# Optimization experiments

Measured on AMD Instinct MI355X. Metric: run time of the kernel, lower is better.

## Reference

```python
import jax, jax.numpy as jnp
import numpy as np

LN_EPS = 1e-5


def _layernorm(x, g, b):
    mu = x.mean(-1, keepdims=True)
    var = x.var(-1, keepdims=True)
    return (x - mu) / jnp.sqrt(var + LN_EPS) * g + b


def _rel_pos_index(p):
    # static numpy computation, identical to the torch buffer
    coords = np.stack(np.meshgrid(np.arange(p), np.arange(p), indexing='ij'))  # (2,p,p)
    flat = coords.reshape(2, -1)  # (2, p*p)
    rel = flat[:, :, None] - flat[:, None, :]  # (2, N, N)
    rel = rel.transpose(1, 2, 0).copy()
    rel[:, :, 0] += p - 1
    rel[:, :, 1] += p - 1
    rel[:, :, 0] *= 2 * p - 1
    return rel.sum(-1)  # (N, N)


def setup_inputs() -> dict:
    key = jax.random.key(0)
    ks = jax.random.split(key, 8)
    B, H, W, C, heads, p = 32, 56, 56, 384, 12, 7
    hid = 4 * C
    s = 0.02
    return {
        'x': jax.random.normal(ks[0], (B, H * W, C), jnp.float32),
        'norm1_g': jnp.ones((C,), jnp.float32),
        'norm1_b': jnp.zeros((C,), jnp.float32),
        'qkv_w': jax.random.normal(ks[1], (3 * C, C), jnp.float32) * s,
        'qkv_b': jnp.zeros((3 * C,), jnp.float32),
        'rpb_table': jax.random.normal(ks[2], ((2 * p - 1) ** 2, heads), jnp.float32) * s,
        'proj_w': jax.random.normal(ks[3], (C, C), jnp.float32) * s,
        'proj_b': jnp.zeros((C,), jnp.float32),
        'norm2_g': jnp.ones((C,), jnp.float32),
        'norm2_b': jnp.zeros((C,), jnp.float32),
        'fc1_w': jax.random.normal(ks[4], (hid, C), jnp.float32) * s,
        'fc1_b': jnp.zeros((hid,), jnp.float32),
        'fc2_w': jax.random.normal(ks[5], (C, hid), jnp.float32) * s,
        'fc2_b': jnp.zeros((C,), jnp.float32),
        'H': H, 'W': W, 'patch_size': p, 'num_heads': heads,
    }


def reference(x, norm1_g, norm1_b, qkv_w, qkv_b, rpb_table, proj_w, proj_b,
              norm2_g, norm2_b, fc1_w, fc1_b, fc2_w, fc2_b,
              H, W, patch_size, num_heads):
    B, L, C = x.shape
    p = patch_size
    N = p * p
    head_dim = C // num_heads
    scale = head_dim ** -0.5

    shortcut = x
    h = _layernorm(x, norm1_g, norm1_b).reshape(B, H, W, C)
    # partition into (B*nWin, N, C); H, W divisible by p so no padding
    h = h.reshape(B, H // p, p, W // p, p, C).transpose(0, 1, 3, 2, 4, 5)
    patches = h.reshape(-1, N, C)
    Bw = patches.shape[0]

    # IPSA attention
    qkv = patches @ qkv_w.T + qkv_b  # (Bw, N, 3C)
    qkv = qkv.reshape(Bw, N, 3, num_heads, head_dim).transpose(2, 0, 3, 1, 4)
    q, k, v = qkv[0] * scale, qkv[1], qkv[2]  # (Bw, h, N, d)
    attn = jnp.einsum('bhnd,bhmd->bhnm', q, k)
    bias = rpb_table[_rel_pos_index(p).reshape(-1)].reshape(N, N, num_heads)
    attn = attn + bias.transpose(2, 0, 1)[None]
    attn = jax.nn.softmax(attn, axis=-1)
    out = jnp.einsum('bhnm,bhmd->bhnd', attn, v).transpose(0, 2, 1, 3).reshape(Bw, N, C)
    out = out @ proj_w.T + proj_b

    # reverse partition
    out = out.reshape(B, H // p, W // p, p, p, C).transpose(0, 1, 3, 2, 4, 5)
    out = out.reshape(B, H * W, C)

    x = shortcut + out
    y = _layernorm(x, norm2_g, norm2_b)
    y = jax.nn.gelu(y @ fc1_w.T + fc1_b, approximate=False)
    y = y @ fc2_w.T + fc2_b
    return x + y
```

## Files before the change

### kernel.cpp

```cpp
#include <hip/hip_runtime.h>
#include <cstdint>
#include <cstddef>

typedef __bf16 bf16;
typedef __bf16 bf16x4 __attribute__((ext_vector_type(4)));
typedef __bf16 bf16x8 __attribute__((ext_vector_type(8)));
typedef float f32x4 __attribute__((ext_vector_type(4)));

static_assert(sizeof(bf16x8) == 16, "bf16x8 must be 16B");

#define NTOK 100352
#define CDIM 384

#define AS1(p) ((const __attribute__((address_space(1))) void*)(p))
#define AS3(p) ((__attribute__((address_space(3))) void*)(p))

__global__ __launch_bounds__(256) void cvt_k(const float* __restrict__ in,
                                             bf16* __restrict__ out, int n)
{
    const int i = (blockIdx.x * 256 + threadIdx.x) * 4;
    if (i < n) {
        const float4 v = *(const float4*)(in + i);
        bf16x4 o;
        o[0] = (bf16)v.x; o[1] = (bf16)v.y; o[2] = (bf16)v.z; o[3] = (bf16)v.w;
        *(bf16x4*)(out + i) = o;
    }
}

__global__ __launch_bounds__(256) void bias_k(const float* __restrict__ rpb,
                                              float* __restrict__ biasE)
{
    const int t = blockIdx.x * 256 + threadIdx.x;
    const int i = t & 63, j = (t >> 6) & 63, hd = t >> 12;
    float v = -3e38f;
    if (i < 49 && j < 49) {
        const int iy = i / 7, ix = i % 7, jy = j / 7, jx = j % 7;
        v = rpb[((jy - iy + 6) * 13 + (jx - ix + 6)) * 12 + hd];
    }
    biasE[t] = v;
}

__global__ __launch_bounds__(256) void ln32_k(const float* __restrict__ x,
    const float* __restrict__ g, const float* __restrict__ b, bf16* __restrict__ y)
{
    const int wave = threadIdx.x >> 6, lane = threadIdx.x & 63;
    const size_t row = (size_t)blockIdx.x * 4 + wave;
    const float2* xr = (const float2*)(x + row * CDIM);
    float v[6];
    float s = 0.f, s2 = 0.f;
#pragma unroll
    for (int i = 0; i < 3; i++) {
        const float2 t = xr[lane + i * 64];
        v[2 * i] = t.x; v[2 * i + 1] = t.y;
        s += t.x + t.y; s2 += t.x * t.x + t.y * t.y;
    }
#pragma unroll
    for (int off = 32; off > 0; off >>= 1) {
        s  += __shfl_xor(s, off);
        s2 += __shfl_xor(s2, off);
    }
    const float mu   = s * (1.f / CDIM);
    const float rstd = rsqrtf(s2 * (1.f / CDIM) - mu * mu + 1e-5f);
    const float2* gu = (const float2*)g;
    const float2* bu = (const float2*)b;
    uint32_t* yu = (uint32_t*)(y + row * CDIM);
#pragma unroll
    for (int i = 0; i < 3; i++) {
        const float2 gg = gu[lane + i * 64], bb = bu[lane + i * 64];
        const float o0 = (v[2 * i] - mu) * rstd * gg.x + bb.x;
        const float o1 = (v[2 * i + 1] - mu) * rstd * gg.y + bb.y;
        const uint32_t pk = (uint32_t)__builtin_bit_cast(unsigned short, (bf16)o0)
                          | ((uint32_t)__builtin_bit_cast(unsigned short, (bf16)o1) << 16);
        yu[lane + i * 64] = pk;
    }
}

template <int EPI, typename TO>
__global__ __launch_bounds__(256) void gemm_bt(
    const bf16* __restrict__ A, const bf16* __restrict__ Bm,
    const float* __restrict__ bias, const float* __restrict__ res,
    TO* __restrict__ Cc, int N, int K)
{
    __shared__ __align__(16) bf16 lds[2][2][128 * 32];
    const int tid = threadIdx.x;

    const int gx = gridDim.x;
    const int nwg = gx * gridDim.y;
    const int orig = blockIdx.y * gx + blockIdx.x;
    const int q = nwg >> 3, r = nwg & 7;
    const int xcd = orig & 7, lid = orig >> 3;
    const int swz = (xcd < r ? xcd * (q + 1) : r * (q + 1) + (xcd - r) * q) + lid;
    const int m0 = (swz / gx) * 128, n0 = (swz % gx) * 128;

    const int wave = tid >> 6, lane = tid & 63;
    const int wm = (wave >> 1) * 64, wn = (wave & 1) * 64;
    const int lm = lane & 15, lk = (lane >> 4) * 8;

    const int sr = tid >> 2;
    const int sc = (tid & 3) * 8;

    const bf16* Ap0 = A + (size_t)(m0 + sr) * K + sc;
    const bf16* Ap1 = A + (size_t)(m0 + sr + 64) * K + sc;
    const bf16* Bp0 = Bm + (size_t)(n0 + sr) * K + sc;
    const bf16* Bp1 = Bm + (size_t)(n0 + sr + 64) * K + sc;

#define STAGE(buf, koff) do {                                                           \
    __builtin_amdgcn_global_load_lds(AS1(Ap0 + (koff)),                                 \
        AS3(&lds[buf][0][(wave * 16) * 32]), 16, 0, 0);                                 \
    __builtin_amdgcn_global_load_lds(AS1(Ap1 + (koff)),                                 \
        AS3(&lds[buf][0][(64 + wave * 16) * 32]), 16, 0, 0);                            \
    __builtin_amdgcn_global_load_lds(AS1(Bp0 + (koff)),                                 \
        AS3(&lds[buf][1][(wave * 16) * 32]), 16, 0, 0);                                 \
    __builtin_amdgcn_global_load_lds(AS1(Bp1 + (koff)),                                 \
        AS3(&lds[buf][1][(64 + wave * 16) * 32]), 16, 0, 0);                            \
} while (0)

    f32x4 acc[4][4] = {};

    const int nt = K >> 5;
    STAGE(0, 0);
    __syncthreads();
    int cur = 0;
    for (int t = 0; t < nt; ++t) {
        const bool more = (t + 1 < nt);
        if (more) STAGE(cur ^ 1, (t + 1) << 5);
        bf16x8 af[4], bfr[4];
#pragma unroll
        for (int i = 0; i < 4; i++)
            af[i] = *(const bf16x8*)&lds[cur][0][(wm + i * 16 + lm) * 32 + lk];
#pragma unroll
        for (int i = 0; i < 4; i++)
            bfr[i] = *(const bf16x8*)&lds[cur][1][(wn + i * 16 + lm) * 32 + lk];
#pragma unroll
        for (int mi = 0; mi < 4; mi++)
#pragma unroll
            for (int ni = 0; ni < 4; ni++)
                acc[mi][ni] = __builtin_amdgcn_mfma_f32_16x16x32_bf16(
                    af[mi], bfr[ni], acc[mi][ni], 0, 0, 0);
        if (more) { __syncthreads(); cur ^= 1; }
    }
#undef STAGE

    if (EPI == 2) {
        const int rb = m0 + wm + (lane >> 4) * 4;
        const int cb = n0 + wn + lm;
#pragma unroll
        for (int ni = 0; ni < 4; ni++) {
            const int col = cb + ni * 16;
            const float bv = bias[col];
#pragma unroll
            for (int mi = 0; mi < 4; mi++) {
#pragma unroll
                for (int r2 = 0; r2 < 4; r2++) {
                    const int row = rb + mi * 16 + r2;
                    float v = acc[mi][ni][r2] + bv;
                    v += res[(size_t)row * N + col];
                    Cc[(size_t)row * N + col] = (TO)v;
                }
            }
        }
    } else {
        __syncthreads();
        bf16* Ct = (bf16*)lds;
        const int rbl = wm + (lane >> 4) * 4;
        const int cbl = wn + lm;
#pragma unroll
        for (int ni = 0; ni < 4; ni++) {
            const float bv = bias[n0 + cbl + ni * 16];
#pragma unroll
            for (int mi = 0; mi < 4; mi++) {
#pragma unroll
                for (int r2 = 0; r2 < 4; r2++) {
                    float v = acc[mi][ni][r2] + bv;
                    if (EPI == 1) {
                        const float p  = fmaf(v * v, 0.07135481627f, 1.59576912161f);
                        const float u2 = fminf(v * p, 80.f);
                        const float e  = __expf(u2);
                        v = v * e * __builtin_amdgcn_rcpf(1.f + e);
                    }
                    Ct[(rbl + mi * 16 + r2) * 128 + cbl + ni * 16] = (bf16)v;
                }
            }
        }
        __syncthreads();
#pragma unroll
        for (int c2 = 0; c2 < 8; ++c2) {
            const int chunk = tid + (c2 << 8);
            const int row = chunk >> 4, c8 = (chunk & 15) << 3;
            *(bf16x8*)((bf16*)Cc + (size_t)(m0 + row) * N + n0 + c8) =
                *(const bf16x8*)&Ct[row * 128 + c8];
        }
    }
}

__global__ __launch_bounds__(256) void attn_k(const bf16* __restrict__ qkv,
    const float* __restrict__ biasE, bf16* __restrict__ out)
{
    const int w  = blockIdx.x;
    const int bb = w >> 6, win = w & 63, wy = win >> 3, wx = win & 7;
    __shared__ int toks[64];
    __shared__ __align__(16) bf16 VT[4][32 * 64];
    __shared__ __align__(16) bf16 P[4][64 * 64];
    const int tid = threadIdx.x;
    if (tid < 64) {
        const int t = tid < 49 ? tid : 48;
        toks[tid] = bb * 3136 + (wy * 7 + t / 7) * 56 + wx * 7 + t % 7;
    }
    __syncthreads();

    const int wave = tid >> 6, lane = tid & 63;
    const int g = lane >> 4, lr = lane & 15;
    char* vt = (char*)VT[wave];
    char* pb = (char*)P[wave];

    for (int hh = 0; hh < 3; ++hh) {
        const int hd = wave * 3 + hh;
#pragma unroll
        for (int c = 0; c < 4; ++c) {
            const int idx = c * 64 + lane;
            const int row = idx >> 2, d0 = (idx & 3) * 8;
            if (row < 49) {
                const bf16x8 vv = *(const bf16x8*)(qkv + (size_t)toks[row] * 1152 + 768 + hd * 32 + d0);
#pragma unroll
                for (int e = 0; e < 8; ++e) {
                    const int d = d0 + e;
                    *(bf16*)(vt + (((d * 64 + row) * 2) ^ ((d & 7) << 4))) = vv[e];
                }
            } else {
#pragma unroll
                for (int e = 0; e < 8; ++e) {
                    const int d = d0 + e;
                    *(bf16*)(vt + (((d * 64 + row) * 2) ^ ((d & 7) << 4))) = (bf16)0.f;
                }
            }
        }
        bf16x8 kf[4], qf[4];
#pragma unroll
        for (int b = 0; b < 4; ++b) {
            const size_t rk = (size_t)toks[b * 16 + lr] * 1152;
            kf[b] = *(const bf16x8*)(qkv + rk + 384 + hd * 32 + g * 8);
            qf[b] = *(const bf16x8*)(qkv + rk +       hd * 32 + g * 8);
        }
        f32x4 s[4][4] = {};
#pragma unroll
        for (int mi = 0; mi < 4; ++mi)
#pragma unroll
            for (int nj = 0; nj < 4; ++nj)
                s[mi][nj] = __builtin_amdgcn_mfma_f32_16x16x32_bf16(kf[mi], qf[nj], s[mi][nj], 0, 0, 0);
        const float* bh = biasE + hd * 4096;
#pragma unroll
        for (int nj = 0; nj < 4; ++nj) {
            const int j = nj * 16 + lr;
            const float* bj = bh + j * 64 + g * 4;
            float mx = -3e38f;
#pragma unroll
            for (int mi = 0; mi < 4; ++mi) {
                const float4 be = *(const float4*)(bj + mi * 16);
                const float* bp4 = (const float*)&be;
#pragma unroll
                for (int r2 = 0; r2 < 4; ++r2) {
                    const float v = fmaf(s[mi][nj][r2], 0.1767766952966369f, bp4[r2]);
                    s[mi][nj][r2] = v;
                    mx = fmaxf(mx, v);
                }
            }
            mx = fmaxf(mx, __shfl_xor(mx, 16));
            mx = fmaxf(mx, __shfl_xor(mx, 32));
            float sm = 0.f;
#pragma unroll
            for (int mi = 0; mi < 4; ++mi)
#pragma unroll
                for (int r2 = 0; r2 < 4; ++r2) {
                    const float e = __expf(s[mi][nj][r2] - mx);
                    s[mi][nj][r2] = e;
                    sm += e;
                }
            sm += __shfl_xor(sm, 16);
            sm += __shfl_xor(sm, 32);
            const float inv = __builtin_amdgcn_rcpf(sm);
#pragma unroll
            for (int mi = 0; mi < 4; ++mi) {
                bf16x4 pk;
#pragma unroll
                for (int r2 = 0; r2 < 4; ++r2) pk[r2] = (bf16)(s[mi][nj][r2] * inv);
                const int i0 = mi * 16 + g * 4;
                *(bf16x4*)(pb + (((j * 64 + i0) * 2) ^ ((j & 7) << 4))) = pk;
            }
        }
        f32x4 o[2][4] = {};
#pragma unroll
        for (int kb = 0; kb < 2; ++kb) {
            bf16x8 av[2], bp[4];
#pragma unroll
            for (int db = 0; db < 2; ++db) {
                const int d = db * 16 + lr;
                av[db] = *(const bf16x8*)(vt + (((d * 64 + kb * 32 + g * 8) * 2) ^ ((d & 7) << 4)));
            }
#pragma unroll
            for (int jb = 0; jb < 4; ++jb) {
                const int j = jb * 16 + lr;
                bp[jb] = *(const bf16x8*)(pb + (((j * 64 + kb * 32 + g * 8) * 2) ^ ((j & 7) << 4)));
            }
#pragma unroll
            for (int db = 0; db < 2; ++db)
#pragma unroll
                for (int jb = 0; jb < 4; ++jb)
                    o[db][jb] = __builtin_amdgcn_mfma_f32_16x16x32_bf16(av[db], bp[jb], o[db][jb], 0, 0, 0);
        }
#pragma unroll
        for (int jb = 0; jb < 4; ++jb) {
            const int j = jb * 16 + lr;
            if (j < 49) {
                bf16* op = out + (size_t)toks[j] * CDIM + hd * 32 + g * 4;
#pragma unroll
                for (int db = 0; db < 2; ++db) {
                    bf16x4 pk;
#pragma unroll
                    for (int r2 = 0; r2 < 4; ++r2) pk[r2] = (bf16)o[db][jb][r2];
                    *(bf16x4*)(op + db * 16) = pk;
                }
            }
        }
    }
}

extern "C" void kernel_launch(void* const* d_in, const int* in_sizes, int n_in,
                              void* d_out, int out_size, void* d_ws, size_t ws_size,
                              hipStream_t stream) {
    const float* x      = (const float*)d_in[0];
    const float* n1g    = (const float*)d_in[1];
    const float* n1b    = (const float*)d_in[2];
    const float* qkv_w  = (const float*)d_in[3];
    const float* qkv_b  = (const float*)d_in[4];
    const float* rpb    = (const float*)d_in[5];
    const float* proj_w = (const float*)d_in[6];
    const float* proj_b = (const float*)d_in[7];
    const float* n2g    = (const float*)d_in[8];
    const float* n2b    = (const float*)d_in[9];
    const float* fc1_w  = (const float*)d_in[10];
    const float* fc1_b  = (const float*)d_in[11];
    const float* fc2_w  = (const float*)d_in[12];
    const float* fc2_b  = (const float*)d_in[13];
    float* out = (float*)d_out;

    const size_t wBytes = 3538944 + 196608;
    int nc = 16;
    for (int c : {1, 2, 4, 8}) {
        if (wBytes + ((size_t)NTOK / c) * 3840 <= ws_size) { nc = c; break; }
    }
    const int rowsC = NTOK / nc;
    const int imgsC = 32 / nc;

    char* ws = (char*)d_ws;
    bf16* wqkv  = (bf16*)ws;
    bf16* wproj = wqkv + 442368;
    bf16* wfc1  = wproj + 147456;
    bf16* wfc2  = wfc1 + 589824;
    float* biasE = (float*)(ws + 3538944);
    bf16* bufH  = (bf16*)(ws + wBytes);
    bf16* bufB  = bufH + (size_t)rowsC * CDIM;
    float* x1   = out;

    cvt_k<<<442368 / 1024, 256, 0, stream>>>(qkv_w, wqkv, 442368);
    cvt_k<<<147456 / 1024, 256, 0, stream>>>(proj_w, wproj, 147456);
    cvt_k<<<589824 / 1024, 256, 0, stream>>>(fc1_w, wfc1, 589824);
    cvt_k<<<589824 / 1024, 256, 0, stream>>>(fc2_w, wfc2, 589824);
    bias_k<<<192, 256, 0, stream>>>(rpb, biasE);

    for (int c = 0; c < nc; c++) {
        const size_t ro = (size_t)c * rowsC;
        ln32_k<<<rowsC / 4, 256, 0, stream>>>(x + ro * CDIM, n1g, n1b, bufH);
        gemm_bt<0, bf16><<<dim3(1152 / 128, rowsC / 128), 256, 0, stream>>>(
            bufH, wqkv, qkv_b, nullptr, bufB, 1152, 384);
        attn_k<<<dim3(64 * imgsC), 256, 0, stream>>>(bufB, biasE, bufH);
        gemm_bt<2, float><<<dim3(384 / 128, rowsC / 128), 256, 0, stream>>>(
            bufH, wproj, proj_b, x + ro * CDIM, x1 + ro * CDIM, 384, 384);
    }
    for (int c = 0; c < nc; c++) {
        const size_t ro = (size_t)c * rowsC;
        ln32_k<<<rowsC / 4, 256, 0, stream>>>(x1 + ro * CDIM, n2g, n2b, bufH);
        gemm_bt<1, bf16><<<dim3(1536 / 128, rowsC / 128), 256, 0, stream>>>(
            bufH, wfc1, fc1_b, nullptr, bufB, 1536, 384);
        gemm_bt<2, float><<<dim3(384 / 128, rowsC / 128), 256, 0, stream>>>(
            bufB, wfc2, fc2_b, x1 + ro * CDIM, out + ro * CDIM, 384, 1536);
    }
}
```

Before: 1.116 ms.

## Triple-buffer GEMM LDS staging with XOR swizzle to avoid bank conflicts

Moves the bf16 GEMM from double to triple buffering in LDS. Loads are issued two K-tiles ahead, and explicit vmcnt waits plus raw s_barrier replace __syncthreads. It also XOR-swizzles the 16-byte column chunks within each LDS row, on both the global_load_lds write and the fragment read, to reduce LDS bank conflicts. The aim is to hide global load latency and cut LDS read stalls, at the cost of 50% more LDS per block (possible occupancy loss) and hand-tuned waitcnt counts that must match the loads issued.

```diff
diff --git a/kernel.cpp b/kernel.cpp
--- a/kernel.cpp
+++ b/kernel.cpp
@@ -81,7 +81,7 @@
     const float* __restrict__ bias, const float* __restrict__ res,
     TO* __restrict__ Cc, int N, int K)
 {
-    __shared__ __align__(16) bf16 lds[2][2][128 * 32];
+    __shared__ __align__(16) bf16 lds[3][2][128 * 32];
     const int tid = threadIdx.x;
 
     const int gx = gridDim.x;
@@ -94,10 +94,11 @@
 
     const int wave = tid >> 6, lane = tid & 63;
     const int wm = (wave >> 1) * 64, wn = (wave & 1) * 64;
-    const int lm = lane & 15, lk = (lane >> 4) * 8;
+    const int lm = lane & 15;
+    const int lko = (((lane >> 4) ^ ((lm >> 1) & 3)) & 3) * 8;
 
     const int sr = tid >> 2;
-    const int sc = (tid & 3) * 8;
+    const int sc = (((tid & 3) ^ ((sr >> 1) & 3)) & 3) * 8;
 
     const bf16* Ap0 = A + (size_t)(m0 + sr) * K + sc;
     const bf16* Ap1 = A + (size_t)(m0 + sr + 64) * K + sc;
@@ -119,25 +120,38 @@
 
     const int nt = K >> 5;
     STAGE(0, 0);
-    __syncthreads();
-    int cur = 0;
+    STAGE(1, 32);
+    int bi = 0;
     for (int t = 0; t < nt; ++t) {
-        const bool more = (t + 1 < nt);
-        if (more) STAGE(cur ^ 1, (t + 1) << 5);
+        if (t + 2 < nt) {
+            const int b2 = bi ? bi - 1 : 2;
+            STAGE(b2, (t + 2) << 5);
+            asm volatile("s_waitcnt vmcnt(8)" ::: "memory");
+        } else if (t + 1 < nt) {
+            asm volatile("s_waitcnt vmcnt(4)" ::: "memory");
+        } else {
+            asm volatile("s_waitcnt vmcnt(0)" ::: "memory");
+        }
+        __builtin_amdgcn_sched_barrier(0);
+        __builtin_amdgcn_s_barrier();
         bf16x8 af[4], bfr[4];
 #pragma unroll
         for (int i = 0; i < 4; i++)
-            af[i] = *(const bf16x8*)&lds[cur][0][(wm + i * 16 + lm) * 32 + lk];
+            af[i] = *(const bf16x8*)&lds[bi][0][(wm + i * 16 + lm) * 32 + lko];
 #pragma unroll
         for (int i = 0; i < 4; i++)
-            bfr[i] = *(const bf16x8*)&lds[cur][1][(wn + i * 16 + lm) * 32 + lk];
+            bfr[i] = *(const bf16x8*)&lds[bi][1][(wn + i * 16 + lm) * 32 + lko];
 #pragma unroll
         for (int mi = 0; mi < 4; mi++)
 #pragma unroll
             for (int ni = 0; ni < 4; ni++)
                 acc[mi][ni] = __builtin_amdgcn_mfma_f32_16x16x32_bf16(
                     af[mi], bfr[ni], acc[mi][ni], 0, 0, 0);
-        if (more) { __syncthreads(); cur ^= 1; }
+        if (t + 1 < nt) {
+            __builtin_amdgcn_sched_barrier(0);
+            __builtin_amdgcn_s_barrier();
+        }
+        bi = (bi == 2) ? 0 : bi + 1;
     }
 #undef STAGE
 
```

Measured after the change: 1.079 ms. -3.3%, faster.
